# Optimization experiments

Hardware: AMD Instinct MI355X
Metric: run time of the kernel (lower is better)

Reference implementation:

```python
import jax, jax.numpy as jnp
import numpy as np

T, B, IN, H, OUT, L = 2048, 128, 64, 128, 32, 2


def setup_inputs() -> dict:
    key = jax.random.key(0)
    ks = jax.random.split(key, 8)
    s_in = 1.0 / np.sqrt(H)  # torch LSTM init scale: U(-1/sqrt(H), 1/sqrt(H))
    inp = {
        "x": jax.random.normal(ks[0], (T, B, IN), dtype=jnp.float32),
        "w_ih0": jax.random.uniform(ks[1], (4 * H, IN), minval=-s_in, maxval=s_in, dtype=jnp.float32),
        "w_hh0": jax.random.uniform(ks[2], (4 * H, H), minval=-s_in, maxval=s_in, dtype=jnp.float32),
        "w_ih1": jax.random.uniform(ks[3], (4 * H, H), minval=-s_in, maxval=s_in, dtype=jnp.float32),
        "w_hh1": jax.random.uniform(ks[4], (4 * H, H), minval=-s_in, maxval=s_in, dtype=jnp.float32),
        "fc_w": jax.random.uniform(ks[5], (OUT, H), minval=-s_in, maxval=s_in, dtype=jnp.float32),
        "fc_b": jax.random.uniform(ks[6], (OUT,), minval=-s_in, maxval=s_in, dtype=jnp.float32),
    }
    return inp


def _lstm_layer(x, w_ih, w_hh):
    # x: [T, B, D]; gate order i, f, g, o (PyTorch convention), no bias.
    x_proj = jnp.einsum("tbd,gd->tbg", x, w_ih)  # [T, B, 4H] precomputed input GEMM
    h0 = jnp.zeros((x.shape[1], H), dtype=x.dtype)
    c0 = jnp.zeros((x.shape[1], H), dtype=x.dtype)

    def step(carry, xp):
        h, c = carry
        gates = xp + h @ w_hh.T  # [B, 4H]
        i, f, g, o = jnp.split(gates, 4, axis=-1)
        i = jax.nn.sigmoid(i)
        f = jax.nn.sigmoid(f)
        g = jnp.tanh(g)
        o = jax.nn.sigmoid(o)
        c = f * c + i * g
        h = o * jnp.tanh(c)
        return (h, c), h

    (h_n, c_n), ys = jax.lax.scan(step, (h0, c0), x_proj)
    return ys, h_n, c_n


def reference(x, w_ih0, w_hh0, w_ih1, w_hh1, fc_w, fc_b):
    y0, h0n, c0n = _lstm_layer(x, w_ih0, w_hh0)
    y1, h1n, c1n = _lstm_layer(y0, w_ih1, w_hh1)
    out = jnp.einsum("tbh,oh->tbo", y1, fc_w) + fc_b  # [T, B, OUT]
    h_n = jnp.stack([h0n, h1n], axis=0)  # [L, B, H]
    c_n = jnp.stack([c0n, c1n], axis=0)
    return out, (h_n, c_n)
```

## Files before the change

### kernel.cpp

```cpp
#include <hip/hip_runtime.h>

#define T_ 2048
#define B_ 128
#define IN_ 64
#define H_ 128
#define OUT_ 32
#define CH_ 32
#define RING_ 2

typedef _Float16 half8 __attribute__((ext_vector_type(8)));
typedef _Float16 half4v __attribute__((ext_vector_type(4)));
typedef float float4v __attribute__((ext_vector_type(4)));

#define XSTR 144
#define HSTR 272
#define GRP_ELEMS ((size_t)RING_ * CH_ * 16 * 128)
#define RING_BYTES ((size_t)8 * GRP_ELEMS * 2)

__device__ __forceinline__ float sigm(float x) {
  return __builtin_amdgcn_rcpf(1.0f + __expf(-x));
}
__device__ __forceinline__ float tanh_f(float x) {
  return fmaf(-2.0f, __builtin_amdgcn_rcpf(1.0f + __expf(2.0f * x)), 1.0f);
}

__device__ __forceinline__ half8 make_afrag(const float* __restrict__ W, int K, int row, int col) {
  const float* p = W + (size_t)row * K + col;
  float4 a = *(const float4*)p;
  float4 b = *(const float4*)(p + 4);
  half8 h;
  h[0]=(_Float16)a.x; h[1]=(_Float16)a.y; h[2]=(_Float16)a.z; h[3]=(_Float16)a.w;
  h[4]=(_Float16)b.x; h[5]=(_Float16)b.y; h[6]=(_Float16)b.z; h[7]=(_Float16)b.w;
  return h;
}

__device__ __forceinline__ void wait_ge(int* p, int want) {
  while (__hip_atomic_load(p, __ATOMIC_RELAXED, __HIP_MEMORY_SCOPE_AGENT) < want)
    __builtin_amdgcn_s_sleep(2);
}

__global__ void ring_init(int* f) { if (threadIdx.x < 16) f[threadIdx.x] = 0; }

__global__ __launch_bounds__(512) void lstm_wavefront(
    const float* __restrict__ x, const float* __restrict__ w_ih0,
    const float* __restrict__ w_hh0, const float* __restrict__ w_ih1,
    const float* __restrict__ w_hh1, const float* __restrict__ fc_w,
    const float* __restrict__ fc_b, float* __restrict__ out, char* __restrict__ ws)
{
  const int tid  = threadIdx.x, lane = tid & 63, w = tid >> 6;
  const int quad = lane >> 4, n = lane & 15;
  const int g = blockIdx.x & 7, layer = blockIdx.x >> 3;
  _Float16* ring = (_Float16*)ws + (size_t)g * GRP_ELEMS;
  int* flag     = (int*)(ws + RING_BYTES) + g;
  int* consumed = (int*)(ws + RING_BYTES) + 8 + g;

  __shared__ char sh_x[2 * 16 * XSTR];
  __shared__ char sh_h[2 * 16 * HSTR];

  const size_t hn_base = (size_t)T_ * B_ * OUT_;
  float4v c = {0.f, 0.f, 0.f, 0.f};
  float hf[4] = {0.f, 0.f, 0.f, 0.f};

  for (int i = tid; i < 2 * 16 * HSTR / 4; i += 512) ((unsigned*)sh_h)[i] = 0u;

  if (layer == 0) {
    half8 a_x[4][2], a_h[4][4];
#pragma unroll
    for (int gt = 0; gt < 4; ++gt) {
      const int row = gt * H_ + w * 16 + n;
#pragma unroll
      for (int kt = 0; kt < 2; ++kt) a_x[gt][kt] = make_afrag(w_ih0, IN_, row, kt * 32 + quad * 8);
#pragma unroll
      for (int kt = 0; kt < 4; ++kt) a_h[gt][kt] = make_afrag(w_hh0, H_, row, kt * 32 + quad * 8);
    }
    {
      const int xn = tid >> 5, xk = (tid & 31) * 2;
      float2 xv = *(const float2*)(x + ((size_t)0 * B_ + g * 16 + xn) * IN_ + xk);
      _Float16* d = (_Float16*)(sh_x + xn * XSTR + xk * 2);
      d[0] = (_Float16)xv.x; d[1] = (_Float16)xv.y;
    }
    __syncthreads();
    int p = 0;
    half4v hh_def = {0, 0, 0, 0};

    for (int t = 0; t < T_; ++t) {
      const int ck = t >> 5, s = t & (CH_ - 1);
      if (s == 0 && ck >= RING_) wait_ge(consumed, ck - 1);
      if (t > 0) {
        const int tp = t - 1;
        *(half4v*)(ring + ((size_t)(((tp >> 5) % RING_) * CH_ + (tp & (CH_ - 1))) * 16 + n) * 128
                   + w * 16 + quad * 4) = hh_def;
      }
      const int xn = tid >> 5, xk = (tid & 31) * 2;
      float2 xv = make_float2(0.f, 0.f);
      if (t + 1 < T_) xv = *(const float2*)(x + ((size_t)(t + 1) * B_ + g * 16 + xn) * IN_ + xk);

      half8 Bx[2], Bh[4];
#pragma unroll
      for (int kt = 0; kt < 2; ++kt)
        Bx[kt] = *(const half8*)(sh_x + (t & 1) * 16 * XSTR + n * XSTR + (kt * 32 + quad * 8) * 2);
#pragma unroll
      for (int kt = 0; kt < 4; ++kt)
        Bh[kt] = *(const half8*)(sh_h + p * 16 * HSTR + n * HSTR + (kt * 32 + quad * 8) * 2);

      float4 act[4];
#pragma unroll
      for (int gt = 0; gt < 4; ++gt) {
        float4v acc = {0.f, 0.f, 0.f, 0.f};
        acc = __builtin_amdgcn_mfma_f32_16x16x32_f16(a_x[gt][0], Bx[0], acc, 0, 0, 0);
        acc = __builtin_amdgcn_mfma_f32_16x16x32_f16(a_x[gt][1], Bx[1], acc, 0, 0, 0);
#pragma unroll
        for (int kt = 0; kt < 4; ++kt)
          acc = __builtin_amdgcn_mfma_f32_16x16x32_f16(a_h[gt][kt], Bh[kt], acc, 0, 0, 0);
        if (gt == 2) act[gt] = make_float4(tanh_f(acc[0]), tanh_f(acc[1]), tanh_f(acc[2]), tanh_f(acc[3]));
        else         act[gt] = make_float4(sigm(acc[0]), sigm(acc[1]), sigm(acc[2]), sigm(acc[3]));
      }
      half4v hh;
      {
        const float* iv = &act[0].x; const float* fv = &act[1].x;
        const float* gv = &act[2].x; const float* ov = &act[3].x;
#pragma unroll
        for (int r = 0; r < 4; ++r) {
          c[r] = fv[r] * c[r] + iv[r] * gv[r];
          hf[r] = ov[r] * tanh_f(c[r]);
          hh[r] = (_Float16)hf[r];
        }
      }
      *(half4v*)(sh_h + (1 - p) * 16 * HSTR + n * HSTR + (w * 16 + quad * 4) * 2) = hh;
      hh_def = hh;
      if (t + 1 < T_) {
        _Float16* d = (_Float16*)(sh_x + ((t + 1) & 1) * 16 * XSTR + xn * XSTR + xk * 2);
        d[0] = (_Float16)xv.x; d[1] = (_Float16)xv.y;
      }
      __syncthreads();
      if (tid == 0 && s == 0 && t > 0) {
        __builtin_amdgcn_fence(__ATOMIC_RELEASE, "agent");
        __hip_atomic_store(flag, ck, __ATOMIC_RELAXED, __HIP_MEMORY_SCOPE_AGENT);
      }
      p ^= 1;
    }
    {
      const int tp = T_ - 1;
      *(half4v*)(ring + ((size_t)(((tp >> 5) % RING_) * CH_ + (tp & (CH_ - 1))) * 16 + n) * 128
                 + w * 16 + quad * 4) = hh_def;
    }
    __syncthreads();
    if (tid == 0) {
      __builtin_amdgcn_fence(__ATOMIC_RELEASE, "agent");
      __hip_atomic_store(flag, T_ / CH_, __ATOMIC_RELAXED, __HIP_MEMORY_SCOPE_AGENT);
    }
    {
      float* hn = out + hn_base;
      float* cn = out + hn_base + 2 * (size_t)B_ * H_;
      size_t idx = (size_t)(g * 16 + n) * H_ + w * 16 + quad * 4;
      *(float4*)(hn + idx) = make_float4(hf[0], hf[1], hf[2], hf[3]);
      *(float4*)(cn + idx) = make_float4(c[0], c[1], c[2], c[3]);
    }
  } else {
    half8 a_i[4][4], a_h[4][4], a_fc[4];
#pragma unroll
    for (int gt = 0; gt < 4; ++gt) {
      const int row = gt * H_ + w * 16 + n;
#pragma unroll
      for (int kt = 0; kt < 4; ++kt) {
        a_i[gt][kt] = make_afrag(w_ih1, H_, row, kt * 32 + quad * 8);
        a_h[gt][kt] = make_afrag(w_hh1, H_, row, kt * 32 + quad * 8);
      }
    }
    float4 fb = make_float4(0.f, 0.f, 0.f, 0.f);
    if (w < 2) {
#pragma unroll
      for (int kt = 0; kt < 4; ++kt) a_fc[kt] = make_afrag(fc_w, H_, w * 16 + n, kt * 32 + quad * 8);
      fb = *(const float4*)(fc_b + w * 16 + quad * 4);
    }
    __syncthreads();
    int q = 0;
    half8 By[4];

    for (int t = 0; t < T_; ++t) {
      const int ck = t >> 5, s = t & (CH_ - 1);
      if (s == 0) {
        wait_ge(flag, ck + 1);
        __builtin_amdgcn_fence(__ATOMIC_ACQUIRE, "agent");
        const _Float16* yp = ring + ((size_t)((ck % RING_) * CH_) * 16 + n) * 128 + quad * 8;
#pragma unroll
        for (int kt = 0; kt < 4; ++kt) By[kt] = *(const half8*)(yp + kt * 32);
      }
      half8 Bh[4];
#pragma unroll
      for (int kt = 0; kt < 4; ++kt)
        Bh[kt] = *(const half8*)(sh_h + q * 16 * HSTR + n * HSTR + (kt * 32 + quad * 8) * 2);
      if (w < 2 && t > 0) {
        float4v af = {0.f, 0.f, 0.f, 0.f};
#pragma unroll
        for (int kt = 0; kt < 4; ++kt)
          af = __builtin_amdgcn_mfma_f32_16x16x32_f16(a_fc[kt], Bh[kt], af, 0, 0, 0);
        float* op = out + ((size_t)(t - 1) * B_ + g * 16 + n) * OUT_ + w * 16 + quad * 4;
        *(float4*)op = make_float4(af[0] + fb.x, af[1] + fb.y, af[2] + fb.z, af[3] + fb.w);
      }
      float4 act[4];
#pragma unroll
      for (int gt = 0; gt < 4; ++gt) {
        float4v acc = {0.f, 0.f, 0.f, 0.f};
#pragma unroll
        for (int kt = 0; kt < 4; ++kt)
          acc = __builtin_amdgcn_mfma_f32_16x16x32_f16(a_i[gt][kt], By[kt], acc, 0, 0, 0);
#pragma unroll
        for (int kt = 0; kt < 4; ++kt)
          acc = __builtin_amdgcn_mfma_f32_16x16x32_f16(a_h[gt][kt], Bh[kt], acc, 0, 0, 0);
        if (gt == 2) act[gt] = make_float4(tanh_f(acc[0]), tanh_f(acc[1]), tanh_f(acc[2]), tanh_f(acc[3]));
        else         act[gt] = make_float4(sigm(acc[0]), sigm(acc[1]), sigm(acc[2]), sigm(acc[3]));
      }
      half8 Byn[4];
      const bool pf = (s != CH_ - 1) && (t + 1 < T_);
      if (pf) {
        const _Float16* yp = ring + ((size_t)((ck % RING_) * CH_ + s + 1) * 16 + n) * 128 + quad * 8;
#pragma unroll
        for (int kt = 0; kt < 4; ++kt) Byn[kt] = *(const half8*)(yp + kt * 32);
      }
      half4v hh;
      {
        const float* iv = &act[0].x; const float* fv = &act[1].x;
        const float* gv = &act[2].x; const float* ov = &act[3].x;
#pragma unroll
        for (int r = 0; r < 4; ++r) {
          c[r] = fv[r] * c[r] + iv[r] * gv[r];
          hf[r] = ov[r] * tanh_f(c[r]);
          hh[r] = (_Float16)hf[r];
        }
      }
      *(half4v*)(sh_h + (1 - q) * 16 * HSTR + n * HSTR + (w * 16 + quad * 4) * 2) = hh;
      __syncthreads();
      if (s == CH_ - 1 && tid == 0) {
        __builtin_amdgcn_fence(__ATOMIC_RELEASE, "agent");
        __hip_atomic_store(consumed, ck + 1, __ATOMIC_RELAXED, __HIP_MEMORY_SCOPE_AGENT);
      }
      if (pf) {
#pragma unroll
        for (int kt = 0; kt < 4; ++kt) By[kt] = Byn[kt];
      }
      q ^= 1;
    }
    if (w < 2) {
      float4v af = {0.f, 0.f, 0.f, 0.f};
#pragma unroll
      for (int kt = 0; kt < 4; ++kt) {
        half8 Bh = *(const half8*)(sh_h + q * 16 * HSTR + n * HSTR + (kt * 32 + quad * 8) * 2);
        af = __builtin_amdgcn_mfma_f32_16x16x32_f16(a_fc[kt], Bh, af, 0, 0, 0);
      }
      float* op = out + ((size_t)(T_ - 1) * B_ + g * 16 + n) * OUT_ + w * 16 + quad * 4;
      *(float4*)op = make_float4(af[0] + fb.x, af[1] + fb.y, af[2] + fb.z, af[3] + fb.w);
    }
    {
      float* hn = out + hn_base + (size_t)B_ * H_;
      float* cn = out + hn_base + 3 * (size_t)B_ * H_;
      size_t idx = (size_t)(g * 16 + n) * H_ + w * 16 + quad * 4;
      *(float4*)(hn + idx) = make_float4(hf[0], hf[1], hf[2], hf[3]);
      *(float4*)(cn + idx) = make_float4(c[0], c[1], c[2], c[3]);
    }
  }
}

extern "C" void kernel_launch(void* const* d_in, const int* in_sizes, int n_in,
                              void* d_out, int out_size, void* d_ws, size_t ws_size,
                              hipStream_t stream) {
  const float* x     = (const float*)d_in[0];
  const float* w_ih0 = (const float*)d_in[1];
  const float* w_hh0 = (const float*)d_in[2];
  const float* w_ih1 = (const float*)d_in[3];
  const float* w_hh1 = (const float*)d_in[4];
  const float* fc_w  = (const float*)d_in[5];
  const float* fc_b  = (const float*)d_in[6];
  char* ws = (char*)d_ws;
  ring_init<<<1, 64, 0, stream>>>((int*)(ws + RING_BYTES));
  lstm_wavefront<<<16, 512, 0, stream>>>(x, w_ih0, w_hh0, w_ih1, w_hh1,
                                         fc_w, fc_b, (float*)d_out, ws);
}
```

Baseline: 3.079 ms.

## Precompute next-step input projection off the recurrence path and batch FC output

Both layers now compute the input-projection MFMAs for step t+1 after the current step's recurrent MFMAs, so only the h-dependent MFMAs sit on the serial critical path. Gate weights are pre-scaled by -log2e or 2log2e so the activations can use hardware exp2 directly. The h buffer becomes an 8-deep LDS ring, which lets the layer-1 FC projection run every 4 steps spread over all 8 waves instead of on 2 waves every step. The cost is more LDS and registers, plus a small precision change from folding the scale factors into the fp16 weights.

```diff
diff --git a/kernel.cpp b/kernel.cpp
--- a/kernel.cpp
+++ b/kernel.cpp
@@ -17,20 +17,44 @@
 #define GRP_ELEMS ((size_t)RING_ * CH_ * 16 * 128)
 #define RING_BYTES ((size_t)8 * GRP_ELEMS * 2)
 
-__device__ __forceinline__ float sigm(float x) {
-  return __builtin_amdgcn_rcpf(1.0f + __expf(-x));
-}
-__device__ __forceinline__ float tanh_f(float x) {
-  return fmaf(-2.0f, __builtin_amdgcn_rcpf(1.0f + __expf(2.0f * x)), 1.0f);
-}
-
-__device__ __forceinline__ half8 make_afrag(const float* __restrict__ W, int K, int row, int col) {
+#define NLOG2E  (-1.4426950408889634f)
+#define C2LOG2E ( 2.8853900817779268f)
+
+__device__ __forceinline__ float exp2_hw(float x) {
+#if __has_builtin(__builtin_amdgcn_exp2f)
+  return __builtin_amdgcn_exp2f(x);
+#else
+  return exp2f(x);
+#endif
+}
+__device__ __forceinline__ float sigm_pre(float xs) {
+  return __builtin_amdgcn_rcpf(1.0f + exp2_hw(xs));
+}
+__device__ __forceinline__ float tanh_pre(float xs) {
+  return fmaf(-2.0f, __builtin_amdgcn_rcpf(1.0f + exp2_hw(xs)), 1.0f);
+}
+__device__ __forceinline__ float tanh_c(float x) { return tanh_pre(x * C2LOG2E); }
+
+__device__ __forceinline__ float4v sigm4(float4v a) {
+  float4v r;
+#pragma unroll
+  for (int i = 0; i < 4; ++i) r[i] = sigm_pre(a[i]);
+  return r;
+}
+__device__ __forceinline__ float4v tanh4(float4v a) {
+  float4v r;
+#pragma unroll
+  for (int i = 0; i < 4; ++i) r[i] = tanh_pre(a[i]);
+  return r;
+}
+
+__device__ __forceinline__ half8 make_afrag(const float* __restrict__ W, int K, int row, int col, float sc) {
   const float* p = W + (size_t)row * K + col;
   float4 a = *(const float4*)p;
   float4 b = *(const float4*)(p + 4);
   half8 h;
-  h[0]=(_Float16)a.x; h[1]=(_Float16)a.y; h[2]=(_Float16)a.z; h[3]=(_Float16)a.w;
-  h[4]=(_Float16)b.x; h[5]=(_Float16)b.y; h[6]=(_Float16)b.z; h[7]=(_Float16)b.w;
+  h[0]=(_Float16)(a.x*sc); h[1]=(_Float16)(a.y*sc); h[2]=(_Float16)(a.z*sc); h[3]=(_Float16)(a.w*sc);
+  h[4]=(_Float16)(b.x*sc); h[5]=(_Float16)(b.y*sc); h[6]=(_Float16)(b.z*sc); h[7]=(_Float16)(b.w*sc);
   return h;
 }
 
@@ -54,82 +78,98 @@
   int* flag     = (int*)(ws + RING_BYTES) + g;
   int* consumed = (int*)(ws + RING_BYTES) + 8 + g;
 
-  __shared__ char sh_x[2 * 16 * XSTR];
-  __shared__ char sh_h[2 * 16 * HSTR];
+  __shared__ char sh_x[4 * 16 * XSTR];
+  __shared__ char sh_h[8 * 16 * HSTR];
 
   const size_t hn_base = (size_t)T_ * B_ * OUT_;
   float4v c = {0.f, 0.f, 0.f, 0.f};
   float hf[4] = {0.f, 0.f, 0.f, 0.f};
 
-  for (int i = tid; i < 2 * 16 * HSTR / 4; i += 512) ((unsigned*)sh_h)[i] = 0u;
+  for (int i = tid; i < 8 * 16 * HSTR / 4; i += 512) ((unsigned*)sh_h)[i] = 0u;
 
   if (layer == 0) {
     half8 a_x[4][2], a_h[4][4];
 #pragma unroll
     for (int gt = 0; gt < 4; ++gt) {
+      const float sc = (gt == 2) ? C2LOG2E : NLOG2E;
       const int row = gt * H_ + w * 16 + n;
 #pragma unroll
-      for (int kt = 0; kt < 2; ++kt) a_x[gt][kt] = make_afrag(w_ih0, IN_, row, kt * 32 + quad * 8);
-#pragma unroll
-      for (int kt = 0; kt < 4; ++kt) a_h[gt][kt] = make_afrag(w_hh0, H_, row, kt * 32 + quad * 8);
-    }
+      for (int kt = 0; kt < 2; ++kt) a_x[gt][kt] = make_afrag(w_ih0, IN_, row, kt * 32 + quad * 8, sc);
+#pragma unroll
+      for (int kt = 0; kt < 4; ++kt) a_h[gt][kt] = make_afrag(w_hh0, H_, row, kt * 32 + quad * 8, sc);
+    }
+    const int xn = tid >> 5, xk = (tid & 31) * 2;
     {
-      const int xn = tid >> 5, xk = (tid & 31) * 2;
-      float2 xv = *(const float2*)(x + ((size_t)0 * B_ + g * 16 + xn) * IN_ + xk);
-      _Float16* d = (_Float16*)(sh_x + xn * XSTR + xk * 2);
-      d[0] = (_Float16)xv.x; d[1] = (_Float16)xv.y;
+#pragma unroll
+      for (int k = 0; k < 2; ++k) {
+        float2 xv = *(const float2*)(x + ((size_t)k * B_ + g * 16 + xn) * IN_ + xk);
+        _Float16* d = (_Float16*)(sh_x + k * 16 * XSTR + xn * XSTR + xk * 2);
+        d[0] = (_Float16)xv.x; d[1] = (_Float16)xv.y;
+      }
     }
     __syncthreads();
-    int p = 0;
+    float4v accI[4];
+    {
+      half8 Bx[2];
+#pragma unroll
+      for (int kt = 0; kt < 2; ++kt)
+        Bx[kt] = *(const half8*)(sh_x + n * XSTR + (kt * 32 + quad * 8) * 2);
+#pragma unroll
+      for (int gt = 0; gt < 4; ++gt) {
+        float4v a0 = {0.f, 0.f, 0.f, 0.f};
+        a0 = __builtin_amdgcn_mfma_f32_16x16x32_f16(a_x[gt][0], Bx[0], a0, 0, 0, 0);
+        a0 = __builtin_amdgcn_mfma_f32_16x16x32_f16(a_x[gt][1], Bx[1], a0, 0, 0, 0);
+        accI[gt] = a0;
+      }
+    }
     half4v hh_def = {0, 0, 0, 0};
 
     for (int t = 0; t < T_; ++t) {
       const int ck = t >> 5, s = t & (CH_ - 1);
       if (s == 0 && ck >= RING_) wait_ge(consumed, ck - 1);
-      if (t > 0) {
-        const int tp = t - 1;
-        *(half4v*)(ring + ((size_t)(((tp >> 5) % RING_) * CH_ + (tp & (CH_ - 1))) * 16 + n) * 128
-                   + w * 16 + quad * 4) = hh_def;
-      }
-      const int xn = tid >> 5, xk = (tid & 31) * 2;
+      if (t > 0)
+        *(half4v*)(ring + ((size_t)((t - 1) & 63) * 16 + n) * 128 + w * 16 + quad * 4) = hh_def;
       float2 xv = make_float2(0.f, 0.f);
-      if (t + 1 < T_) xv = *(const float2*)(x + ((size_t)(t + 1) * B_ + g * 16 + xn) * IN_ + xk);
-
-      half8 Bx[2], Bh[4];
-#pragma unroll
-      for (int kt = 0; kt < 2; ++kt)
-        Bx[kt] = *(const half8*)(sh_x + (t & 1) * 16 * XSTR + n * XSTR + (kt * 32 + quad * 8) * 2);
+      if (t + 2 < T_) xv = *(const float2*)(x + ((size_t)(t + 2) * B_ + g * 16 + xn) * IN_ + xk);
+
+      half8 Bh[4];
 #pragma unroll
       for (int kt = 0; kt < 4; ++kt)
-        Bh[kt] = *(const half8*)(sh_h + p * 16 * HSTR + n * HSTR + (kt * 32 + quad * 8) * 2);
-
-      float4 act[4];
+        Bh[kt] = *(const half8*)(sh_h + ((t - 1) & 7) * 16 * HSTR + n * HSTR + (kt * 32 + quad * 8) * 2);
+
+      float4v ga[4];
 #pragma unroll
       for (int gt = 0; gt < 4; ++gt) {
-        float4v acc = {0.f, 0.f, 0.f, 0.f};
-        acc = __builtin_amdgcn_mfma_f32_16x16x32_f16(a_x[gt][0], Bx[0], acc, 0, 0, 0);
-        acc = __builtin_amdgcn_mfma_f32_16x16x32_f16(a_x[gt][1], Bx[1], acc, 0, 0, 0);
+        float4v acc = accI[gt];
 #pragma unroll
         for (int kt = 0; kt < 4; ++kt)
           acc = __builtin_amdgcn_mfma_f32_16x16x32_f16(a_h[gt][kt], Bh[kt], acc, 0, 0, 0);
-        if (gt == 2) act[gt] = make_float4(tanh_f(acc[0]), tanh_f(acc[1]), tanh_f(acc[2]), tanh_f(acc[3]));
-        else         act[gt] = make_float4(sigm(acc[0]), sigm(acc[1]), sigm(acc[2]), sigm(acc[3]));
+        ga[gt] = (gt == 2) ? tanh4(acc) : sigm4(acc);
+      }
+      if (t + 1 < T_) {
+        half8 Bx[2];
+#pragma unroll
+        for (int kt = 0; kt < 2; ++kt)
+          Bx[kt] = *(const half8*)(sh_x + ((t + 1) & 3) * 16 * XSTR + n * XSTR + (kt * 32 + quad * 8) * 2);
+#pragma unroll
+        for (int gt = 0; gt < 4; ++gt) {
+          float4v a0 = {0.f, 0.f, 0.f, 0.f};
+          a0 = __builtin_amdgcn_mfma_f32_16x16x32_f16(a_x[gt][0], Bx[0], a0, 0, 0, 0);
+          a0 = __builtin_amdgcn_mfma_f32_16x16x32_f16(a_x[gt][1], Bx[1], a0, 0, 0, 0);
+          accI[gt] = a0;
+        }
       }
       half4v hh;
-      {
-        const float* iv = &act[0].x; const float* fv = &act[1].x;
-        const float* gv = &act[2].x; const float* ov = &act[3].x;
-#pragma unroll
-        for (int r = 0; r < 4; ++r) {
-          c[r] = fv[r] * c[r] + iv[r] * gv[r];
-          hf[r] = ov[r] * tanh_f(c[r]);
-          hh[r] = (_Float16)hf[r];
-        }
-      }
-      *(half4v*)(sh_h + (1 - p) * 16 * HSTR + n * HSTR + (w * 16 + quad * 4) * 2) = hh;
+#pragma unroll
+      for (int r = 0; r < 4; ++r) {
+        c[r] = fmaf(ga[1][r], c[r], ga[0][r] * ga[2][r]);
+        hf[r] = ga[3][r] * tanh_c(c[r]);
+        hh[r] = (_Float16)hf[r];
+      }
+      *(half4v*)(sh_h + (t & 7) * 16 * HSTR + n * HSTR + (w * 16 + quad * 4) * 2) = hh;
       hh_def = hh;
-      if (t + 1 < T_) {
-        _Float16* d = (_Float16*)(sh_x + ((t + 1) & 1) * 16 * XSTR + xn * XSTR + xk * 2);
+      if (t + 2 < T_) {
+        _Float16* d = (_Float16*)(sh_x + ((t + 2) & 3) * 16 * XSTR + xn * XSTR + xk * 2);
         d[0] = (_Float16)xv.x; d[1] = (_Float16)xv.y;
       }
       __syncthreads();
@@ -137,13 +177,8 @@
         __builtin_amdgcn_fence(__ATOMIC_RELEASE, "agent");
         __hip_atomic_store(flag, ck, __ATOMIC_RELAXED, __HIP_MEMORY_SCOPE_AGENT);
       }
-      p ^= 1;
-    }
-    {
-      const int tp = T_ - 1;
-      *(half4v*)(ring + ((size_t)(((tp >> 5) % RING_) * CH_ + (tp & (CH_ - 1))) * 16 + n) * 128
-                 + w * 16 + quad * 4) = hh_def;
-    }
+    }
+    *(half4v*)(ring + ((size_t)((T_ - 1) & 63) * 16 + n) * 128 + w * 16 + quad * 4) = hh_def;
     __syncthreads();
     if (tid == 0) {
       __builtin_amdgcn_fence(__ATOMIC_RELEASE, "agent");
@@ -160,96 +195,96 @@
     half8 a_i[4][4], a_h[4][4], a_fc[4];
 #pragma unroll
     for (int gt = 0; gt < 4; ++gt) {
+      const float sc = (gt == 2) ? C2LOG2E : NLOG2E;
       const int row = gt * H_ + w * 16 + n;
 #pragma unroll
       for (int kt = 0; kt < 4; ++kt) {
-        a_i[gt][kt] = make_afrag(w_ih1, H_, row, kt * 32 + quad * 8);
-        a_h[gt][kt] = make_afrag(w_hh1, H_, row, kt * 32 + quad * 8);
-      }
-    }
-    float4 fb = make_float4(0.f, 0.f, 0.f, 0.f);
-    if (w < 2) {
-#pragma unroll
-      for (int kt = 0; kt < 4; ++kt) a_fc[kt] = make_afrag(fc_w, H_, w * 16 + n, kt * 32 + quad * 8);
-      fb = *(const float4*)(fc_b + w * 16 + quad * 4);
-    }
+        a_i[gt][kt] = make_afrag(w_ih1, H_, row, kt * 32 + quad * 8, sc);
+        a_h[gt][kt] = make_afrag(w_hh1, H_, row, kt * 32 + quad * 8, sc);
+      }
+    }
+#pragma unroll
+    for (int kt = 0; kt < 4; ++kt)
+      a_fc[kt] = make_afrag(fc_w, H_, (w & 1) * 16 + n, kt * 32 + quad * 8, 1.0f);
+    const float4 fb = *(const float4*)(fc_b + (w & 1) * 16 + quad * 4);
     __syncthreads();
-    int q = 0;
-    half8 By[4];
+
+    float4v accI[4];
+#pragma unroll
+    for (int gt = 0; gt < 4; ++gt) accI[gt] = (float4v){0.f, 0.f, 0.f, 0.f};
 
     for (int t = 0; t < T_; ++t) {
       const int ck = t >> 5, s = t & (CH_ - 1);
       if (s == 0) {
         wait_ge(flag, ck + 1);
         __builtin_amdgcn_fence(__ATOMIC_ACQUIRE, "agent");
-        const _Float16* yp = ring + ((size_t)((ck % RING_) * CH_) * 16 + n) * 128 + quad * 8;
+        const _Float16* yp = ring + ((size_t)(t & 63) * 16 + n) * 128 + quad * 8;
+        half8 By[4];
 #pragma unroll
         for (int kt = 0; kt < 4; ++kt) By[kt] = *(const half8*)(yp + kt * 32);
+#pragma unroll
+        for (int gt = 0; gt < 4; ++gt) {
+          float4v a0 = {0.f, 0.f, 0.f, 0.f};
+#pragma unroll
+          for (int kt = 0; kt < 4; ++kt)
+            a0 = __builtin_amdgcn_mfma_f32_16x16x32_f16(a_i[gt][kt], By[kt], a0, 0, 0, 0);
+          accI[gt] = a0;
+        }
       }
       half8 Bh[4];
 #pragma unroll
       for (int kt = 0; kt < 4; ++kt)
-        Bh[kt] = *(const half8*)(sh_h + q * 16 * HSTR + n * HSTR + (kt * 32 + quad * 8) * 2);
-      if (w < 2 && t > 0) {
-        float4v af = {0.f, 0.f, 0.f, 0.f};
-#pragma unroll
-        for (int kt = 0; kt < 4; ++kt)
-          af = __builtin_amdgcn_mfma_f32_16x16x32_f16(a_fc[kt], Bh[kt], af, 0, 0, 0);
-        float* op = out + ((size_t)(t - 1) * B_ + g * 16 + n) * OUT_ + w * 16 + quad * 4;
-        *(float4*)op = make_float4(af[0] + fb.x, af[1] + fb.y, af[2] + fb.z, af[3] + fb.w);
-      }
-      float4 act[4];
+        Bh[kt] = *(const half8*)(sh_h + ((t - 1) & 7) * 16 * HSTR + n * HSTR + (kt * 32 + quad * 8) * 2);
+
+      float4v ga[4];
 #pragma unroll
       for (int gt = 0; gt < 4; ++gt) {
-        float4v acc = {0.f, 0.f, 0.f, 0.f};
-#pragma unroll
-        for (int kt = 0; kt < 4; ++kt)
-          acc = __builtin_amdgcn_mfma_f32_16x16x32_f16(a_i[gt][kt], By[kt], acc, 0, 0, 0);
+        float4v acc = accI[gt];
 #pragma unroll
         for (int kt = 0; kt < 4; ++kt)
           acc = __builtin_amdgcn_mfma_f32_16x16x32_f16(a_h[gt][kt], Bh[kt], acc, 0, 0, 0);
-        if (gt == 2) act[gt] = make_float4(tanh_f(acc[0]), tanh_f(acc[1]), tanh_f(acc[2]), tanh_f(acc[3]));
-        else         act[gt] = make_float4(sigm(acc[0]), sigm(acc[1]), sigm(acc[2]), sigm(acc[3]));
-      }
-      half8 Byn[4];
-      const bool pf = (s != CH_ - 1) && (t + 1 < T_);
-      if (pf) {
-        const _Float16* yp = ring + ((size_t)((ck % RING_) * CH_ + s + 1) * 16 + n) * 128 + quad * 8;
-#pragma unroll
-        for (int kt = 0; kt < 4; ++kt) Byn[kt] = *(const half8*)(yp + kt * 32);
+        ga[gt] = (gt == 2) ? tanh4(acc) : sigm4(acc);
+      }
+      if (s != CH_ - 1) {
+        const _Float16* yp = ring + ((size_t)((t + 1) & 63) * 16 + n) * 128 + quad * 8;
+        half8 By[4];
+#pragma unroll
+        for (int kt = 0; kt < 4; ++kt) By[kt] = *(const half8*)(yp + kt * 32);
+#pragma unroll
+        for (int gt = 0; gt < 4; ++gt) {
+          float4v a0 = {0.f, 0.f, 0.f, 0.f};
+#pragma unroll
+          for (int kt = 0; kt < 4; ++kt)
+            a0 = __builtin_amdgcn_mfma_f32_16x16x32_f16(a_i[gt][kt], By[kt], a0, 0, 0, 0);
+          accI[gt] = a0;
+        }
       }
       half4v hh;
-      {
-        const float* iv = &act[0].x; const float* fv = &act[1].x;
-        const float* gv = &act[2].x; const float* ov = &act[3].x;
-#pragma unroll
-        for (int r = 0; r < 4; ++r) {
-          c[r] = fv[r] * c[r] + iv[r] * gv[r];
-          hf[r] = ov[r] * tanh_f(c[r]);
-          hh[r] = (_Float16)hf[r];
-        }
-      }
-      *(half4v*)(sh_h + (1 - q) * 16 * HSTR + n * HSTR + (w * 16 + quad * 4) * 2) = hh;
+#pragma unroll
+      for (int r = 0; r < 4; ++r) {
+        c[r] = fmaf(ga[1][r], c[r], ga[0][r] * ga[2][r]);
+        hf[r] = ga[3][r] * tanh_c(c[r]);
+        hh[r] = (_Float16)hf[r];
+      }
+      *(half4v*)(sh_h + (t & 7) * 16 * HSTR + n * HSTR + (w * 16 + quad * 4) * 2) = hh;
       __syncthreads();
       if (s == CH_ - 1 && tid == 0) {
         __builtin_amdgcn_fence(__ATOMIC_RELEASE, "agent");
         __hip_atomic_store(consumed, ck + 1, __ATOMIC_RELAXED, __HIP_MEMORY_SCOPE_AGENT);
       }
-      if (pf) {
-#pragma unroll
-        for (int kt = 0; kt < 4; ++kt) By[kt] = Byn[kt];
-      }
-      q ^= 1;
-    }
-    if (w < 2) {
-      float4v af = {0.f, 0.f, 0.f, 0.f};
-#pragma unroll
-      for (int kt = 0; kt < 4; ++kt) {
-        half8 Bh = *(const half8*)(sh_h + q * 16 * HSTR + n * HSTR + (kt * 32 + quad * 8) * 2);
-        af = __builtin_amdgcn_mfma_f32_16x16x32_f16(a_fc[kt], Bh, af, 0, 0, 0);
-      }
-      float* op = out + ((size_t)(T_ - 1) * B_ + g * 16 + n) * OUT_ + w * 16 + quad * 4;
-      *(float4*)op = make_float4(af[0] + fb.x, af[1] + fb.y, af[2] + fb.z, af[3] + fb.w);
+      if ((t & 3) == 3) {
+        const int sj = t - 3 + (w >> 1);
+        half8 Bf[4];
+#pragma unroll
+        for (int kt = 0; kt < 4; ++kt)
+          Bf[kt] = *(const half8*)(sh_h + (sj & 7) * 16 * HSTR + n * HSTR + (kt * 32 + quad * 8) * 2);
+        float4v af = {0.f, 0.f, 0.f, 0.f};
+#pragma unroll
+        for (int kt = 0; kt < 4; ++kt)
+          af = __builtin_amdgcn_mfma_f32_16x16x32_f16(a_fc[kt], Bf[kt], af, 0, 0, 0);
+        float* op = out + ((size_t)sj * B_ + g * 16 + n) * OUT_ + (w & 1) * 16 + quad * 4;
+        *(float4*)op = make_float4(af[0] + fb.x, af[1] + fb.y, af[2] + fb.z, af[3] + fb.w);
+      }
     }
     {
       float* hn = out + hn_base + (size_t)B_ * H_;
```

After: 3.358 ms. 9.1% more time.
